# Kernel tuning notes

Measured on AMD Instinct MI355X. Metric: run time of the kernel, lower is better.

Reference implementation:

```python
import jax, jax.numpy as jnp
import numpy as np

N_NODES, N_EDGES, H = 25000, 400000, 64
EPS = 1e-15


def _norm(x):
    return jnp.sqrt(jnp.sum(x * x, axis=-1, keepdims=True))


def _projx(x, c):
    norm = _norm(x)
    max_norm = (1.0 - 1e-5) / jnp.sqrt(c)
    scale = jnp.minimum(max_norm / jnp.maximum(norm, EPS), 1.0)
    return x * scale


def _expmap0(x, c):
    norm = _norm(x)
    sc = jnp.sqrt(c)
    return jnp.tanh(sc * norm) * x / (norm * sc + EPS)


def _logmap0(x, c):
    norm = _norm(x)
    sc = jnp.sqrt(c)
    return (1.0 / sc) * jnp.arctanh(jnp.minimum(sc * norm, 1.0 - 1e-5)) * x / (norm + EPS)


def _mobius_add(x, y, c):
    x2 = jnp.sum(x * x, axis=-1, keepdims=True)
    y2 = jnp.sum(y * y, axis=-1, keepdims=True)
    xy = jnp.sum(x * y, axis=-1, keepdims=True)
    num = (1.0 + 2.0 * c * xy + c * y2) * x + (1.0 - c * x2) * y
    denom = 1.0 + 2.0 * c * xy + c * c * x2 * y2
    return num / (denom + EPS)


def _mobius_linear(x, W, b, c):
    t = _logmap0(x, c)
    out = t @ W.T + b
    return _expmap0(out, c)


def setup_inputs() -> dict:
    key = jax.random.key(0)
    ks = jax.random.split(key, 12)
    h_V = jax.random.normal(ks[0], (N_NODES, H), dtype=jnp.float32) * 0.3
    h_E = jax.random.normal(ks[1], (N_EDGES, 3 * H), dtype=jnp.float32) * 0.3
    src = jax.random.randint(ks[2], (N_EDGES,), 0, N_NODES, dtype=jnp.int32)
    dst = jax.random.randint(ks[3], (N_EDGES,), 0, N_NODES, dtype=jnp.int32)
    log_c = jnp.zeros((), dtype=jnp.float32)  # c = 1.0

    def lin(k, out_d, in_d):
        bound = 1.0 / np.sqrt(in_d)
        kw, kb = jax.random.split(k)
        W = jax.random.uniform(kw, (out_d, in_d), jnp.float32, -bound, bound)
        b = jax.random.uniform(kb, (out_d,), jnp.float32, -bound, bound)
        return W, b

    W1_w, W1_b = lin(ks[4], H, 5 * H)
    W2_w, W2_b = lin(ks[5], H, H)
    W3_w, W3_b = lin(ks[6], H, H)
    return {"h_V": h_V, "h_E": h_E, "src": src, "dst": dst, "log_c": log_c,
            "W1_w": W1_w, "W1_b": W1_b, "W2_w": W2_w, "W2_b": W2_b,
            "W3_w": W3_w, "W3_b": W3_b}


def reference(h_V, h_E, src, dst, log_c, W1_w, W1_b, W2_w, W2_b, W3_w, W3_b):
    c = jnp.exp(log_c)
    n_nodes = h_V.shape[0]
    h_E = _projx(h_E, c)
    h_V = _projx(h_V, c)
    # edge gather -> fused mobius-linear chain  [E, 5H] -> [E, H]
    h_EV = jnp.concatenate([h_E, h_V[src], h_V[dst]], axis=-1)
    h_EV = _mobius_linear(h_EV, W1_w, W1_b, c)
    h_EV = _mobius_linear(_projx(jax.nn.relu(h_EV), c), W2_w, W2_b, c)
    h_msg = _mobius_linear(_projx(jax.nn.relu(h_EV), c), W3_w, W3_b, c)
    # hyperbolic aggregate: logmap0 -> scatter-mean over src -> expmap0
    tangent = _logmap0(h_msg, c)
    sums = jax.ops.segment_sum(tangent, src, num_segments=n_nodes)
    counts = jax.ops.segment_sum(jnp.ones((tangent.shape[0],), tangent.dtype), src,
                                 num_segments=n_nodes)
    agg_t = sums / jnp.maximum(counts, 1.0)[:, None]
    agg = _expmap0(agg_t, c)
    h_V = _mobius_add(h_V, agg, c)  # dropout disabled (eval)
    return _projx(h_V, c)
```

## Files before the change

### kernel.cpp

```cpp
#include <hip/hip_runtime.h>
#include <hip/hip_bf16.h>
#include <math.h>

#define EPSF 1e-15f

typedef __attribute__((ext_vector_type(8))) short bf16x8;
typedef __attribute__((ext_vector_type(16))) float f32x16;

__device__ __forceinline__ unsigned short f2bf(float x) {
    unsigned u = __float_as_uint(x);
    u += 0x7fffu + ((u >> 16) & 1u);
    return (unsigned short)(u >> 16);
}
__device__ __forceinline__ float bf2f(unsigned short b) {
    return __uint_as_float(((unsigned)b) << 16);
}
__device__ __forceinline__ unsigned pkbf(float lo, float hi) {
    __hip_bfloat162 h = __float22bfloat162_rn(make_float2(lo, hi));
    return *reinterpret_cast<unsigned*>(&h);
}
__device__ __forceinline__ float fast_tanh_pos(float x) {
    if (x < 0.25f) { float x2 = x * x; return x * (1.0f - x2 * (0.33333334f - 0.13333334f * x2)); }
    float e = __expf(2.0f * x);
    return 1.0f - 2.0f / (e + 1.0f);
}
__device__ __forceinline__ float fast_atanh01(float y) {
    if (y < 0.125f) { float y2 = y * y; return y * (1.0f + y2 * (0.33333334f + 0.2f * y2)); }
    return 0.5f * __logf((1.0f + y) / (1.0f - y));
}

__device__ __forceinline__ float wred(float v) {
#pragma unroll
    for (int off = 32; off; off >>= 1) v += __shfl_xor(v, off);
    return v;
}

__global__ void prep_wfrag(const float* __restrict__ W1, const float* __restrict__ W2,
                           const float* __restrict__ W3, unsigned short* __restrict__ Wf) {
    int idx = blockIdx.x * blockDim.x + threadIdx.x;
    if (idx >= 56 * 64) return;
    int fid = idx >> 6, lane = idx & 63;
    int e31 = lane & 31, hi = lane >> 5;
    unsigned short* dstp = Wf + ((size_t)fid * 64 + lane) * 8;
    if (fid < 40) {
        int ks = fid >> 1, t = fid & 1;
        int n = 32 * t + e31;
        int k0 = 16 * ks + 8 * hi;
#pragma unroll
        for (int i = 0; i < 8; ++i) dstp[i] = f2bf(W1[n * 320 + k0 + i]);
    } else {
        const float* srcW = (fid < 48) ? W2 : W3;
        int b = (fid < 48) ? fid - 40 : fid - 48;
        int ks = b >> 1, t2 = b & 1;
        int n = 32 * t2 + e31;
        int cb = 32 * (ks >> 1) + 16 * (ks & 1) + 4 * hi;
#pragma unroll
        for (int i = 0; i < 8; ++i) dstp[i] = f2bf(srcW[n * 64 + cb + 8 * (i >> 2) + (i & 3)]);
    }
}

__global__ void __launch_bounds__(256)
node_prep(const float* __restrict__ hV, const float* __restrict__ logc,
          unsigned short* __restrict__ hVp, float* __restrict__ pj, int n_nodes) {
    int wid  = (blockIdx.x * blockDim.x + threadIdx.x) >> 6;
    int lane = threadIdx.x & 63;
    if (wid >= n_nodes) return;
    float c    = __expf(logc[0]);
    float scq  = sqrtf(c);
    float maxn = (1.0f - 1e-5f) / scq;
    float x = hV[(size_t)wid * 64 + lane];
    float p = wred(x * x);
    float sS = fminf(maxn / fmaxf(sqrtf(p), EPSF), 1.0f);
    hVp[(size_t)wid * 64 + lane] = f2bf(x * sS);
    if (lane == 0) pj[wid] = sS * sS * p;
}

__global__ void hist_kernel(const int* __restrict__ src, int* __restrict__ cnt,
                            int* __restrict__ slot, int n_edges) {
    int e = blockIdx.x * blockDim.x + threadIdx.x;
    if (e < n_edges) slot[e] = atomicAdd(&cnt[src[e]], 1);
}

__global__ void __launch_bounds__(1024)
scan_rowptr(const int* __restrict__ cnt, int* __restrict__ rowptr, int n) {
    __shared__ int wpart[16];
    int C   = (n + 1023) >> 10;
    int tid = threadIdx.x;
    int beg = tid * C;
    int end = beg + C; if (end > n) end = n;
    int s = 0;
    if (beg < n) for (int k = beg; k < end; ++k) s += cnt[k];
    int lane = tid & 63, wv = tid >> 6;
    int v = s;
#pragma unroll
    for (int off = 1; off < 64; off <<= 1) {
        int t = __shfl_up(v, off);
        if (lane >= off) v += t;
    }
    if (lane == 63) wpart[wv] = v;
    __syncthreads();
    if (tid < 64) {
        int t = (tid < 16) ? wpart[tid] : 0;
#pragma unroll
        for (int off = 1; off < 16; off <<= 1) {
            int u = __shfl_up(t, off);
            if (lane >= off) t += u;
        }
        if (tid < 16) wpart[tid] = t;
    }
    __syncthreads();
    int base = (wv ? wpart[wv - 1] : 0) + (v - s);
    if (beg < n) {
        int run = base;
        for (int k = beg; k < end; ++k) { rowptr[k] = run; run += cnt[k]; }
    }
    if (tid == 1023) rowptr[n] = wpart[15];
}

__global__ void slotfix_kernel(const int* __restrict__ src, const int* __restrict__ rowptr,
                               int* __restrict__ slot, int n_edges) {
    int e = blockIdx.x * blockDim.x + threadIdx.x;
    if (e < n_edges) slot[e] += rowptr[src[e]];
}

__device__ __forceinline__ void stage_mlp32(float (&v)[2][16],
                                            const unsigned short* WfL, int fbase,
                                            const float* __restrict__ bvec,
                                            float scq, float maxn, int lane, int hi) {
    float n2 = 0.f, rn2 = 0.f;
    float u[2][16];
#pragma unroll
    for (int t = 0; t < 2; ++t)
#pragma unroll
        for (int j = 0; j < 16; ++j) {
            float x = v[t][j];
            n2 = fmaf(x, x, n2);
            float y = fmaxf(x, 0.f);
            u[t][j] = y;
            rn2 = fmaf(y, y, rn2);
        }
    n2  += __shfl_xor(n2, 32);
    rn2 += __shfl_xor(rn2, 32);
    float n  = sqrtf(n2);
    float h  = fast_tanh_pos(scq * n) / (n * scq + EPSF);
    float rn = h * sqrtf(rn2);
    float ps = fminf(maxn / fmaxf(rn, EPSF), 1.0f);
    float pn = rn * ps;
    float gg = fast_atanh01(fminf(scq * pn, 1.0f - 1e-5f)) / (scq * (pn + EPSF));
    float f2 = h * ps * gg;

    f32x16 acc[2] = {};
#pragma unroll
    for (int ks = 0; ks < 4; ++ks) {
        int t = ks >> 1, jb = 8 * (ks & 1);
        union { bf16x8 b; unsigned w[4]; } B;
        B.w[0] = pkbf(u[t][jb + 0], u[t][jb + 1]);
        B.w[1] = pkbf(u[t][jb + 2], u[t][jb + 3]);
        B.w[2] = pkbf(u[t][jb + 4], u[t][jb + 5]);
        B.w[3] = pkbf(u[t][jb + 6], u[t][jb + 7]);
#pragma unroll
        for (int t2 = 0; t2 < 2; ++t2) {
            bf16x8 wf = *reinterpret_cast<const bf16x8*>(
                &WfL[((fbase + ks * 2 + t2) * 64 + lane) * 8]);
            acc[t2] = __builtin_amdgcn_mfma_f32_32x32x16_bf16(wf, B.b, acc[t2], 0, 0, 0);
        }
    }
#pragma unroll
    for (int t2 = 0; t2 < 2; ++t2)
#pragma unroll
        for (int q = 0; q < 4; ++q) {
            const float4 bv = *reinterpret_cast<const float4*>(&bvec[32 * t2 + 8 * q + 4 * hi]);
            v[t2][4 * q + 0] = fmaf(f2, acc[t2][4 * q + 0], bv.x);
            v[t2][4 * q + 1] = fmaf(f2, acc[t2][4 * q + 1], bv.y);
            v[t2][4 * q + 2] = fmaf(f2, acc[t2][4 * q + 2], bv.z);
            v[t2][4 * q + 3] = fmaf(f2, acc[t2][4 * q + 3], bv.w);
        }
}

__global__ void __launch_bounds__(256, 2)
edge_mfma(const float* __restrict__ hE, const int* __restrict__ src,
          const int* __restrict__ dst, const float* __restrict__ logc,
          const unsigned short* __restrict__ Wf, const unsigned short* __restrict__ hVp,
          const float* __restrict__ pj,
          const float* __restrict__ b1, const float* __restrict__ b2,
          const float* __restrict__ b3, const int* __restrict__ slot,
          unsigned short* __restrict__ tg, int n_edges) {
    __shared__ __align__(16) unsigned short WfL[28672];
    {
        const uint4* wsrc = reinterpret_cast<const uint4*>(Wf);
        uint4* wdst = reinterpret_cast<uint4*>(WfL);
#pragma unroll
        for (int i = 0; i < 14; ++i)
            wdst[i * 256 + threadIdx.x] = wsrc[i * 256 + threadIdx.x];
    }
    __syncthreads();

    int lane = threadIdx.x & 63;
    int w    = threadIdx.x >> 6;
    int tile = blockIdx.x * 4 + w;
    int e0 = tile * 32;
    if (e0 >= n_edges) return;

    float c    = __expf(logc[0]);
    float scq  = sqrtf(c);
    float maxn = (1.0f - 1e-5f) / scq;

    int e31 = lane & 31, hi = lane >> 5;
    int ev = e0 + e31; if (ev >= n_edges) ev = n_edges - 1;
    int s16 = src[ev], d16 = dst[ev];
    float pjS = pj[s16], pjD = pj[d16];
    int sl = slot[ev];

    float4 ha[24];
    const float* eb = hE + (size_t)ev * 192 + 8 * hi;
#pragma unroll
    for (int ks = 0; ks < 12; ++ks) {
        const float4* p4 = reinterpret_cast<const float4*>(eb + 16 * ks);
        ha[2 * ks]     = p4[0];
        ha[2 * ks + 1] = p4[1];
    }
    const bf16x8* vsp = reinterpret_cast<const bf16x8*>(hVp + (size_t)s16 * 64);
    const bf16x8* vdp = reinterpret_cast<const bf16x8*>(hVp + (size_t)d16 * 64);
    bf16x8 aS[4], aD[4];
#pragma unroll
    for (int q = 0; q < 4; ++q) { aS[q] = vsp[2 * q + hi]; aD[q] = vdp[2 * q + hi]; }

    f32x16 accE[2] = {}, accV[2] = {};
    float pE = 0.f;
#pragma unroll
    for (int ks = 0; ks < 12; ++ks) {
        float4 a0 = ha[2 * ks], a1 = ha[2 * ks + 1];
        pE += a0.x*a0.x + a0.y*a0.y + a0.z*a0.z + a0.w*a0.w
            + a1.x*a1.x + a1.y*a1.y + a1.z*a1.z + a1.w*a1.w;
        union { bf16x8 b; unsigned u[4]; } cv;
        cv.u[0] = pkbf(a0.x, a0.y);
        cv.u[1] = pkbf(a0.z, a0.w);
        cv.u[2] = pkbf(a1.x, a1.y);
        cv.u[3] = pkbf(a1.z, a1.w);
#pragma unroll
        for (int t = 0; t < 2; ++t) {
            bf16x8 wf = *reinterpret_cast<const bf16x8*>(&WfL[((ks * 2 + t) * 64 + lane) * 8]);
            accE[t] = __builtin_amdgcn_mfma_f32_32x32x16_bf16(wf, cv.b, accE[t], 0, 0, 0);
        }
    }
#pragma unroll
    for (int q = 0; q < 4; ++q) {
#pragma unroll
        for (int t = 0; t < 2; ++t) {
            bf16x8 wf = *reinterpret_cast<const bf16x8*>(&WfL[(((12 + q) * 2 + t) * 64 + lane) * 8]);
            accV[t] = __builtin_amdgcn_mfma_f32_32x32x16_bf16(wf, aS[q], accV[t], 0, 0, 0);
        }
    }
#pragma unroll
    for (int q = 0; q < 4; ++q) {
#pragma unroll
        for (int t = 0; t < 2; ++t) {
            bf16x8 wf = *reinterpret_cast<const bf16x8*>(&WfL[(((16 + q) * 2 + t) * 64 + lane) * 8]);
            accV[t] = __builtin_amdgcn_mfma_f32_32x32x16_bf16(wf, aD[q], accV[t], 0, 0, 0);
        }
    }

    pE += __shfl_xor(pE, 32);
    float sE = fminf(maxn / fmaxf(sqrtf(pE), EPSF), 1.0f);
    float nt = sqrtf(sE * sE * pE + pjS + pjD);
    float gq = fast_atanh01(fminf(scq * nt, 1.0f - 1e-5f)) / (scq * (nt + EPSF));

    float v[2][16];
#pragma unroll
    for (int t = 0; t < 2; ++t)
#pragma unroll
        for (int q = 0; q < 4; ++q) {
            const float4 bv = *reinterpret_cast<const float4*>(&b1[32 * t + 8 * q + 4 * hi]);
            v[t][4*q+0] = fmaf(gq, fmaf(sE, accE[t][4*q+0], accV[t][4*q+0]), bv.x);
            v[t][4*q+1] = fmaf(gq, fmaf(sE, accE[t][4*q+1], accV[t][4*q+1]), bv.y);
            v[t][4*q+2] = fmaf(gq, fmaf(sE, accE[t][4*q+2], accV[t][4*q+2]), bv.z);
            v[t][4*q+3] = fmaf(gq, fmaf(sE, accE[t][4*q+3], accV[t][4*q+3]), bv.w);
        }

    stage_mlp32(v, WfL, 40, b2, scq, maxn, lane, hi);
    stage_mlp32(v, WfL, 48, b3, scq, maxn, lane, hi);

    float n2 = 0.f;
#pragma unroll
    for (int t = 0; t < 2; ++t)
#pragma unroll
        for (int j = 0; j < 16; ++j) n2 = fmaf(v[t][j], v[t][j], n2);
    n2 += __shfl_xor(n2, 32);
    float n  = sqrtf(n2);
    float h  = fast_tanh_pos(scq * n) / (n * scq + EPSF);
    float hn = h * n;
    float g4 = fast_atanh01(fminf(scq * hn, 1.0f - 1e-5f)) / (scq * (hn + EPSF));
    float fT = g4 * h;

    if (e0 + e31 < n_edges) {
        unsigned short* orow = tg + (size_t)sl * 64;
#pragma unroll
        for (int t = 0; t < 2; ++t)
#pragma unroll
            for (int q = 0; q < 4; ++q) {
                uint2 o;
                o.x = pkbf(fT * v[t][4*q+0], fT * v[t][4*q+1]);
                o.y = pkbf(fT * v[t][4*q+2], fT * v[t][4*q+3]);
                *reinterpret_cast<uint2*>(&orow[32 * t + 8 * q + 4 * hi]) = o;
            }
    }
}

__global__ void __launch_bounds__(256)
node_gather(const float* __restrict__ hV, const float* __restrict__ logc,
            const unsigned short* __restrict__ tg, const int* __restrict__ rowptr,
            float* __restrict__ out, int n_nodes) {
    int wid  = (blockIdx.x * blockDim.x + threadIdx.x) >> 6;
    int lane = threadIdx.x & 63;
    if (wid >= n_nodes) return;

    float c    = __expf(logc[0]);
    float scq  = sqrtf(c);
    float maxn = (1.0f - 1e-5f) / scq;

    int beg = rowptr[wid], end = rowptr[wid + 1];
    int g = lane >> 4, i15 = lane & 15;
    float s0 = 0.f, s1 = 0.f, s2 = 0.f, s3 = 0.f;
    for (int i = beg + g; i < end; i += 4) {
        uint2 p = *reinterpret_cast<const uint2*>(&tg[(size_t)i * 64 + i15 * 4]);
        s0 += bf2f((unsigned short)(p.x & 0xffff));
        s1 += bf2f((unsigned short)(p.x >> 16));
        s2 += bf2f((unsigned short)(p.y & 0xffff));
        s3 += bf2f((unsigned short)(p.y >> 16));
    }
    s0 += __shfl_xor(s0, 16); s0 += __shfl_xor(s0, 32);
    s1 += __shfl_xor(s1, 16); s1 += __shfl_xor(s1, 32);
    s2 += __shfl_xor(s2, 16); s2 += __shfl_xor(s2, 32);
    s3 += __shfl_xor(s3, 16); s3 += __shfl_xor(s3, 32);
    int srcl = lane >> 2;
    float a0 = __shfl(s0, srcl), a1 = __shfl(s1, srcl);
    float a2 = __shfl(s2, srcl), a3 = __shfl(s3, srcl);
    float ssum = (lane & 2) ? ((lane & 1) ? a3 : a2) : ((lane & 1) ? a1 : a0);

    float inv = 1.f / fmaxf((float)(end - beg), 1.f);
    float at  = ssum * inv;

    float an2 = wred(at * at);
    float an  = sqrtf(an2);
    float ae  = fast_tanh_pos(scq * an) / (an * scq + EPSF);

    float xv  = hV[(size_t)wid * 64 + lane];
    float hs2 = wred(xv * xv);
    float sX  = fminf(maxn / fmaxf(sqrtf(hs2), EPSF), 1.0f);

    float x = sX * xv, y = ae * at;
    float x2 = wred(x * x);
    float y2 = wred(y * y);
    float xy = wred(x * y);

    float ca = 1.f + 2.f * c * xy + c * y2;
    float cb = 1.f - c * x2;
    float id = 1.f / (1.f + 2.f * c * xy + c * c * x2 * y2 + EPSF);

    float r   = (ca * x + cb * y) * id;
    float rn2 = wred(r * r);
    float rs  = fminf(maxn / fmaxf(sqrtf(rn2), EPSF), 1.0f);

    out[(size_t)wid * 64 + lane] = rs * r;
}

extern "C" void kernel_launch(void* const* d_in, const int* in_sizes, int n_in,
                              void* d_out, int out_size, void* d_ws, size_t ws_size,
                              hipStream_t stream) {
    const float* hV   = (const float*)d_in[0];
    const float* hE   = (const float*)d_in[1];
    const int*   src  = (const int*)d_in[2];
    const int*   dst  = (const int*)d_in[3];
    const float* logc = (const float*)d_in[4];
    const float* W1   = (const float*)d_in[5];
    const float* b1   = (const float*)d_in[6];
    const float* W2   = (const float*)d_in[7];
    const float* b2   = (const float*)d_in[8];
    const float* W3   = (const float*)d_in[9];
    const float* b3   = (const float*)d_in[10];

    int n_nodes = in_sizes[0] / 64;
    int n_edges = in_sizes[2];
    float* out = (float*)d_out;

    char* wsb = (char*)d_ws;
    unsigned short* Wf = (unsigned short*)wsb;
    size_t off = 56 * 512 * sizeof(unsigned short);
    int* cnt    = (int*)(wsb + off);   off += (size_t)n_nodes * 4;
    int* rowptr = (int*)(wsb + off);   off += (size_t)(n_nodes + 1) * 4;
    int* slot   = (int*)(wsb + off);   off += (size_t)n_edges * 4;
    float* pj   = (float*)(wsb + off); off += (size_t)n_nodes * 4;
    off = (off + 15) & ~(size_t)15;
    unsigned short* hVp = (unsigned short*)(wsb + off);
    off += (size_t)n_nodes * 64 * 2;
    off = (off + 15) & ~(size_t)15;
    unsigned short* tg = (unsigned short*)(wsb + off);

    hipMemsetAsync(cnt, 0, (size_t)n_nodes * sizeof(int), stream);

    prep_wfrag<<<(56 * 64 + 255) / 256, 256, 0, stream>>>(W1, W2, W3, Wf);
    node_prep<<<(n_nodes + 3) / 4, 256, 0, stream>>>(hV, logc, hVp, pj, n_nodes);
    hist_kernel<<<(n_edges + 255) / 256, 256, 0, stream>>>(src, cnt, slot, n_edges);
    scan_rowptr<<<1, 1024, 0, stream>>>(cnt, rowptr, n_nodes);
    slotfix_kernel<<<(n_edges + 255) / 256, 256, 0, stream>>>(src, rowptr, slot, n_edges);

    int tiles = (n_edges + 31) / 32;
    edge_mfma<<<(tiles + 3) / 4, 256, 0, stream>>>(
        hE, src, dst, logc, Wf, hVp, pj, b1, b2, b3, slot, tg, n_edges);

    node_gather<<<(n_nodes + 3) / 4, 256, 0, stream>>>(
        hV, logc, tg, rowptr, out, n_nodes);
}
```

Measured before the change: 220.9 us.

## Make edge kernel persistent with software-pipelined prefetch of next tile

Measured after the change: 295.8 us. 33.9% more time.

```diff
diff --git a/kernel.cpp b/kernel.cpp
--- a/kernel.cpp
+++ b/kernel.cpp
@@ -184,7 +184,7 @@
           const float* __restrict__ pj,
           const float* __restrict__ b1, const float* __restrict__ b2,
           const float* __restrict__ b3, const int* __restrict__ slot,
-          unsigned short* __restrict__ tg, int n_edges) {
+          unsigned short* __restrict__ tg, int n_edges, int n_tiles) {
     __shared__ __align__(16) unsigned short WfL[28672];
     {
         const uint4* wsrc = reinterpret_cast<const uint4*>(Wf);
@@ -197,112 +197,144 @@
 
     int lane = threadIdx.x & 63;
     int w    = threadIdx.x >> 6;
-    int tile = blockIdx.x * 4 + w;
-    int e0 = tile * 32;
-    if (e0 >= n_edges) return;
+    int e31 = lane & 31, hi = lane >> 5;
 
     float c    = __expf(logc[0]);
     float scq  = sqrtf(c);
     float maxn = (1.0f - 1e-5f) / scq;
 
-    int e31 = lane & 31, hi = lane >> 5;
-    int ev = e0 + e31; if (ev >= n_edges) ev = n_edges - 1;
+    int wstride = gridDim.x * 4;
+    int tile = blockIdx.x * 4 + w;
+    if (tile >= n_tiles) return;
+
+    int ev = tile * 32 + e31; if (ev >= n_edges) ev = n_edges - 1;
     int s16 = src[ev], d16 = dst[ev];
+    int sl  = slot[ev];
+    float4 ha[24];
+    {
+        const float* eb = hE + (size_t)ev * 192 + 8 * hi;
+#pragma unroll
+        for (int ks = 0; ks < 12; ++ks) {
+            const float4* p4 = reinterpret_cast<const float4*>(eb + 16 * ks);
+            ha[2 * ks]     = p4[0];
+            ha[2 * ks + 1] = p4[1];
+        }
+    }
+    bf16x8 aS[4], aD[4];
+    {
+        const bf16x8* vsp = reinterpret_cast<const bf16x8*>(hVp + (size_t)s16 * 64);
+        const bf16x8* vdp = reinterpret_cast<const bf16x8*>(hVp + (size_t)d16 * 64);
+#pragma unroll
+        for (int q = 0; q < 4; ++q) { aS[q] = vsp[2 * q + hi]; aD[q] = vdp[2 * q + hi]; }
+    }
     float pjS = pj[s16], pjD = pj[d16];
-    int sl = slot[ev];
-
-    float4 ha[24];
-    const float* eb = hE + (size_t)ev * 192 + 8 * hi;
-#pragma unroll
-    for (int ks = 0; ks < 12; ++ks) {
-        const float4* p4 = reinterpret_cast<const float4*>(eb + 16 * ks);
-        ha[2 * ks]     = p4[0];
-        ha[2 * ks + 1] = p4[1];
-    }
-    const bf16x8* vsp = reinterpret_cast<const bf16x8*>(hVp + (size_t)s16 * 64);
-    const bf16x8* vdp = reinterpret_cast<const bf16x8*>(hVp + (size_t)d16 * 64);
-    bf16x8 aS[4], aD[4];
-#pragma unroll
-    for (int q = 0; q < 4; ++q) { aS[q] = vsp[2 * q + hi]; aD[q] = vdp[2 * q + hi]; }
-
-    f32x16 accE[2] = {}, accV[2] = {};
-    float pE = 0.f;
-#pragma unroll
-    for (int ks = 0; ks < 12; ++ks) {
-        float4 a0 = ha[2 * ks], a1 = ha[2 * ks + 1];
-        pE += a0.x*a0.x + a0.y*a0.y + a0.z*a0.z + a0.w*a0.w
-            + a1.x*a1.x + a1.y*a1.y + a1.z*a1.z + a1.w*a1.w;
-        union { bf16x8 b; unsigned u[4]; } cv;
-        cv.u[0] = pkbf(a0.x, a0.y);
-        cv.u[1] = pkbf(a0.z, a0.w);
-        cv.u[2] = pkbf(a1.x, a1.y);
-        cv.u[3] = pkbf(a1.z, a1.w);
-#pragma unroll
-        for (int t = 0; t < 2; ++t) {
-            bf16x8 wf = *reinterpret_cast<const bf16x8*>(&WfL[((ks * 2 + t) * 64 + lane) * 8]);
-            accE[t] = __builtin_amdgcn_mfma_f32_32x32x16_bf16(wf, cv.b, accE[t], 0, 0, 0);
-        }
-    }
-#pragma unroll
-    for (int q = 0; q < 4; ++q) {
-#pragma unroll
-        for (int t = 0; t < 2; ++t) {
-            bf16x8 wf = *reinterpret_cast<const bf16x8*>(&WfL[(((12 + q) * 2 + t) * 64 + lane) * 8]);
-            accV[t] = __builtin_amdgcn_mfma_f32_32x32x16_bf16(wf, aS[q], accV[t], 0, 0, 0);
-        }
-    }
-#pragma unroll
-    for (int q = 0; q < 4; ++q) {
-#pragma unroll
-        for (int t = 0; t < 2; ++t) {
-            bf16x8 wf = *reinterpret_cast<const bf16x8*>(&WfL[(((16 + q) * 2 + t) * 64 + lane) * 8]);
-            accV[t] = __builtin_amdgcn_mfma_f32_32x32x16_bf16(wf, aD[q], accV[t], 0, 0, 0);
-        }
-    }
-
-    pE += __shfl_xor(pE, 32);
-    float sE = fminf(maxn / fmaxf(sqrtf(pE), EPSF), 1.0f);
-    float nt = sqrtf(sE * sE * pE + pjS + pjD);
-    float gq = fast_atanh01(fminf(scq * nt, 1.0f - 1e-5f)) / (scq * (nt + EPSF));
-
-    float v[2][16];
-#pragma unroll
-    for (int t = 0; t < 2; ++t)
+
+    for (;;) {
+        f32x16 accE[2] = {}, accV[2] = {};
+        float pE = 0.f;
+#pragma unroll
+        for (int ks = 0; ks < 12; ++ks) {
+            float4 a0 = ha[2 * ks], a1 = ha[2 * ks + 1];
+            pE += a0.x*a0.x + a0.y*a0.y + a0.z*a0.z + a0.w*a0.w
+                + a1.x*a1.x + a1.y*a1.y + a1.z*a1.z + a1.w*a1.w;
+            union { bf16x8 b; unsigned u[4]; } cv;
+            cv.u[0] = pkbf(a0.x, a0.y);
+            cv.u[1] = pkbf(a0.z, a0.w);
+            cv.u[2] = pkbf(a1.x, a1.y);
+            cv.u[3] = pkbf(a1.z, a1.w);
+#pragma unroll
+            for (int t = 0; t < 2; ++t) {
+                bf16x8 wf = *reinterpret_cast<const bf16x8*>(&WfL[((ks * 2 + t) * 64 + lane) * 8]);
+                accE[t] = __builtin_amdgcn_mfma_f32_32x32x16_bf16(wf, cv.b, accE[t], 0, 0, 0);
+            }
+        }
 #pragma unroll
         for (int q = 0; q < 4; ++q) {
-            const float4 bv = *reinterpret_cast<const float4*>(&b1[32 * t + 8 * q + 4 * hi]);
-            v[t][4*q+0] = fmaf(gq, fmaf(sE, accE[t][4*q+0], accV[t][4*q+0]), bv.x);
-            v[t][4*q+1] = fmaf(gq, fmaf(sE, accE[t][4*q+1], accV[t][4*q+1]), bv.y);
-            v[t][4*q+2] = fmaf(gq, fmaf(sE, accE[t][4*q+2], accV[t][4*q+2]), bv.z);
-            v[t][4*q+3] = fmaf(gq, fmaf(sE, accE[t][4*q+3], accV[t][4*q+3]), bv.w);
-        }
-
-    stage_mlp32(v, WfL, 40, b2, scq, maxn, lane, hi);
-    stage_mlp32(v, WfL, 48, b3, scq, maxn, lane, hi);
-
-    float n2 = 0.f;
-#pragma unroll
-    for (int t = 0; t < 2; ++t)
-#pragma unroll
-        for (int j = 0; j < 16; ++j) n2 = fmaf(v[t][j], v[t][j], n2);
-    n2 += __shfl_xor(n2, 32);
-    float n  = sqrtf(n2);
-    float h  = fast_tanh_pos(scq * n) / (n * scq + EPSF);
-    float hn = h * n;
-    float g4 = fast_atanh01(fminf(scq * hn, 1.0f - 1e-5f)) / (scq * (hn + EPSF));
-    float fT = g4 * h;
-
-    if (e0 + e31 < n_edges) {
-        unsigned short* orow = tg + (size_t)sl * 64;
+#pragma unroll
+            for (int t = 0; t < 2; ++t) {
+                bf16x8 wf = *reinterpret_cast<const bf16x8*>(&WfL[(((12 + q) * 2 + t) * 64 + lane) * 8]);
+                accV[t] = __builtin_amdgcn_mfma_f32_32x32x16_bf16(wf, aS[q], accV[t], 0, 0, 0);
+            }
+        }
+#pragma unroll
+        for (int q = 0; q < 4; ++q) {
+#pragma unroll
+            for (int t = 0; t < 2; ++t) {
+                bf16x8 wf = *reinterpret_cast<const bf16x8*>(&WfL[(((16 + q) * 2 + t) * 64 + lane) * 8]);
+                accV[t] = __builtin_amdgcn_mfma_f32_32x32x16_bf16(wf, aD[q], accV[t], 0, 0, 0);
+            }
+        }
+
+        pE += __shfl_xor(pE, 32);
+        float sE = fminf(maxn / fmaxf(sqrtf(pE), EPSF), 1.0f);
+        float nt = sqrtf(sE * sE * pE + pjS + pjD);
+        float gq = fast_atanh01(fminf(scq * nt, 1.0f - 1e-5f)) / (scq * (nt + EPSF));
+
+        float v[2][16];
 #pragma unroll
         for (int t = 0; t < 2; ++t)
 #pragma unroll
             for (int q = 0; q < 4; ++q) {
-                uint2 o;
-                o.x = pkbf(fT * v[t][4*q+0], fT * v[t][4*q+1]);
-                o.y = pkbf(fT * v[t][4*q+2], fT * v[t][4*q+3]);
-                *reinterpret_cast<uint2*>(&orow[32 * t + 8 * q + 4 * hi]) = o;
+                const float4 bv = *reinterpret_cast<const float4*>(&b1[32 * t + 8 * q + 4 * hi]);
+                v[t][4*q+0] = fmaf(gq, fmaf(sE, accE[t][4*q+0], accV[t][4*q+0]), bv.x);
+                v[t][4*q+1] = fmaf(gq, fmaf(sE, accE[t][4*q+1], accV[t][4*q+1]), bv.y);
+                v[t][4*q+2] = fmaf(gq, fmaf(sE, accE[t][4*q+2], accV[t][4*q+2]), bv.z);
+                v[t][4*q+3] = fmaf(gq, fmaf(sE, accE[t][4*q+3], accV[t][4*q+3]), bv.w);
             }
+
+        int  sl_cur = sl;
+        bool wr     = (tile * 32 + e31) < n_edges;
+
+        int tile2 = tile + wstride;
+        bool more = tile2 < n_tiles;
+        if (more) {
+            ev = tile2 * 32 + e31; if (ev >= n_edges) ev = n_edges - 1;
+            s16 = src[ev]; d16 = dst[ev]; sl = slot[ev];
+            const float* eb = hE + (size_t)ev * 192 + 8 * hi;
+#pragma unroll
+            for (int ks = 0; ks < 12; ++ks) {
+                const float4* p4 = reinterpret_cast<const float4*>(eb + 16 * ks);
+                ha[2 * ks]     = p4[0];
+                ha[2 * ks + 1] = p4[1];
+            }
+            const bf16x8* vsp = reinterpret_cast<const bf16x8*>(hVp + (size_t)s16 * 64);
+            const bf16x8* vdp = reinterpret_cast<const bf16x8*>(hVp + (size_t)d16 * 64);
+#pragma unroll
+            for (int q = 0; q < 4; ++q) { aS[q] = vsp[2 * q + hi]; aD[q] = vdp[2 * q + hi]; }
+            pjS = pj[s16]; pjD = pj[d16];
+        }
+        __builtin_amdgcn_sched_barrier(0);
+
+        stage_mlp32(v, WfL, 40, b2, scq, maxn, lane, hi);
+        stage_mlp32(v, WfL, 48, b3, scq, maxn, lane, hi);
+
+        float n2 = 0.f;
+#pragma unroll
+        for (int t = 0; t < 2; ++t)
+#pragma unroll
+            for (int j = 0; j < 16; ++j) n2 = fmaf(v[t][j], v[t][j], n2);
+        n2 += __shfl_xor(n2, 32);
+        float n  = sqrtf(n2);
+        float h  = fast_tanh_pos(scq * n) / (n * scq + EPSF);
+        float hn = h * n;
+        float g4 = fast_atanh01(fminf(scq * hn, 1.0f - 1e-5f)) / (scq * (hn + EPSF));
+        float fT = g4 * h;
+
+        if (wr) {
+            unsigned short* orow = tg + (size_t)sl_cur * 64;
+#pragma unroll
+            for (int t = 0; t < 2; ++t)
+#pragma unroll
+                for (int q = 0; q < 4; ++q) {
+                    uint2 o;
+                    o.x = pkbf(fT * v[t][4*q+0], fT * v[t][4*q+1]);
+                    o.y = pkbf(fT * v[t][4*q+2], fT * v[t][4*q+3]);
+                    *reinterpret_cast<uint2*>(&orow[32 * t + 8 * q + 4 * hi]) = o;
+                }
+        }
+
+        if (!more) break;
+        tile = tile2;
     }
 }
 
@@ -404,9 +436,11 @@
     scan_rowptr<<<1, 1024, 0, stream>>>(cnt, rowptr, n_nodes);
     slotfix_kernel<<<(n_edges + 255) / 256, 256, 0, stream>>>(src, rowptr, slot, n_edges);
 
-    int tiles = (n_edges + 31) / 32;
-    edge_mfma<<<(tiles + 3) / 4, 256, 0, stream>>>(
-        hE, src, dst, logc, Wf, hVp, pj, b1, b2, b3, slot, tg, n_edges);
+    int n_tiles = (n_edges + 31) / 32;
+    int nblocks = (n_tiles + 3) / 4;
+    if (nblocks > 512) nblocks = 512;
+    edge_mfma<<<nblocks, 256, 0, stream>>>(
+        hE, src, dst, logc, Wf, hVp, pj, b1, b2, b3, slot, tg, n_edges, n_tiles);
 
     node_gather<<<(n_nodes + 3) / 4, 256, 0, stream>>>(
         hV, logc, tg, rowptr, out, n_nodes);
```

## Split edge-feature GEMM into separate kernel and fold slotfix into edge kernel

Applied to the files above, without the earlier changes.

Result: slower. 526.5 us (+138.3%).

```diff
diff --git a/kernel.cpp b/kernel.cpp
--- a/kernel.cpp
+++ b/kernel.cpp
@@ -117,10 +117,52 @@
     if (tid == 1023) rowptr[n] = wpart[15];
 }
 
-__global__ void slotfix_kernel(const int* __restrict__ src, const int* __restrict__ rowptr,
-                               int* __restrict__ slot, int n_edges) {
-    int e = blockIdx.x * blockDim.x + threadIdx.x;
-    if (e < n_edges) slot[e] += rowptr[src[e]];
+__global__ void __launch_bounds__(256, 8)
+gemm1e(const float* __restrict__ hE, const unsigned short* __restrict__ Wf,
+       unsigned short* __restrict__ yEb, float* __restrict__ pEarr,
+       int n_edges, int n_tiles) {
+    int lane = threadIdx.x & 63;
+    int w    = threadIdx.x >> 6;
+    int tile = blockIdx.x * 4 + w;
+    if (tile >= n_tiles) return;
+    int e31 = lane & 31, hi = lane >> 5;
+    int ev = tile * 32 + e31; if (ev >= n_edges) ev = n_edges - 1;
+
+    const bf16x8* Wfrag = reinterpret_cast<const bf16x8*>(Wf);
+    const float* eb = hE + (size_t)ev * 192 + 8 * hi;
+
+    f32x16 acc[2] = {};
+    float pE = 0.f;
+#pragma unroll
+    for (int ks = 0; ks < 12; ++ks) {
+        const float4* p4 = reinterpret_cast<const float4*>(eb + 16 * ks);
+        float4 a0 = p4[0], a1 = p4[1];
+        pE += a0.x*a0.x + a0.y*a0.y + a0.z*a0.z + a0.w*a0.w
+            + a1.x*a1.x + a1.y*a1.y + a1.z*a1.z + a1.w*a1.w;
+        union { bf16x8 b; unsigned u[4]; } cv;
+        cv.u[0] = pkbf(a0.x, a0.y);
+        cv.u[1] = pkbf(a0.z, a0.w);
+        cv.u[2] = pkbf(a1.x, a1.y);
+        cv.u[3] = pkbf(a1.z, a1.w);
+#pragma unroll
+        for (int t = 0; t < 2; ++t)
+            acc[t] = __builtin_amdgcn_mfma_f32_32x32x16_bf16(
+                Wfrag[(size_t)(ks * 2 + t) * 64 + lane], cv.b, acc[t], 0, 0, 0);
+    }
+    pE += __shfl_xor(pE, 32);
+
+    unsigned pk[16];
+#pragma unroll
+    for (int t = 0; t < 2; ++t)
+#pragma unroll
+        for (int wd = 0; wd < 8; ++wd)
+            pk[t * 8 + wd] = pkbf(acc[t][2 * wd], acc[t][2 * wd + 1]);
+    uint4* op = reinterpret_cast<uint4*>(yEb + ((size_t)tile * 64 + lane) * 32);
+    op[0] = make_uint4(pk[0],  pk[1],  pk[2],  pk[3]);
+    op[1] = make_uint4(pk[4],  pk[5],  pk[6],  pk[7]);
+    op[2] = make_uint4(pk[8],  pk[9],  pk[10], pk[11]);
+    op[3] = make_uint4(pk[12], pk[13], pk[14], pk[15]);
+    if (hi == 0 && tile * 32 + e31 < n_edges) pEarr[tile * 32 + e31] = pE;
 }
 
 __device__ __forceinline__ void stage_mlp32(float (&v)[2][16],
@@ -177,20 +219,22 @@
         }
 }
 
-__global__ void __launch_bounds__(256, 2)
-edge_mfma(const float* __restrict__ hE, const int* __restrict__ src,
-          const int* __restrict__ dst, const float* __restrict__ logc,
+__global__ void __launch_bounds__(256, 4)
+edge_mfma(const unsigned short* __restrict__ yEb, const float* __restrict__ pEarr,
+          const int* __restrict__ src, const int* __restrict__ dst,
+          const float* __restrict__ logc,
           const unsigned short* __restrict__ Wf, const unsigned short* __restrict__ hVp,
           const float* __restrict__ pj,
           const float* __restrict__ b1, const float* __restrict__ b2,
-          const float* __restrict__ b3, const int* __restrict__ slot,
-          unsigned short* __restrict__ tg, int n_edges) {
-    __shared__ __align__(16) unsigned short WfL[28672];
+          const float* __restrict__ b3, const int* __restrict__ slot_,
+          const int* __restrict__ rowptr,
+          unsigned short* __restrict__ tg, int n_edges, int n_tiles) {
+    __shared__ __align__(16) unsigned short WfL[16384];
     {
-        const uint4* wsrc = reinterpret_cast<const uint4*>(Wf);
+        const uint4* wsrc = reinterpret_cast<const uint4*>(Wf) + 1536;
         uint4* wdst = reinterpret_cast<uint4*>(WfL);
 #pragma unroll
-        for (int i = 0; i < 14; ++i)
+        for (int i = 0; i < 8; ++i)
             wdst[i * 256 + threadIdx.x] = wsrc[i * 256 + threadIdx.x];
     }
     __syncthreads();
@@ -198,69 +242,48 @@
     int lane = threadIdx.x & 63;
     int w    = threadIdx.x >> 6;
     int tile = blockIdx.x * 4 + w;
-    int e0 = tile * 32;
-    if (e0 >= n_edges) return;
+    if (tile >= n_tiles) return;
 
     float c    = __expf(logc[0]);
     float scq  = sqrtf(c);
     float maxn = (1.0f - 1e-5f) / scq;
 
     int e31 = lane & 31, hi = lane >> 5;
-    int ev = e0 + e31; if (ev >= n_edges) ev = n_edges - 1;
+    int ev = tile * 32 + e31; if (ev >= n_edges) ev = n_edges - 1;
     int s16 = src[ev], d16 = dst[ev];
+    int sl = slot_[ev] + rowptr[s16];
     float pjS = pj[s16], pjD = pj[d16];
-    int sl = slot[ev];
-
-    float4 ha[24];
-    const float* eb = hE + (size_t)ev * 192 + 8 * hi;
-#pragma unroll
-    for (int ks = 0; ks < 12; ++ks) {
-        const float4* p4 = reinterpret_cast<const float4*>(eb + 16 * ks);
-        ha[2 * ks]     = p4[0];
-        ha[2 * ks + 1] = p4[1];
-    }
+    float pE  = pEarr[ev];
+
+    const uint4* yp = reinterpret_cast<const uint4*>(yEb + ((size_t)tile * 64 + lane) * 32);
+    uint4 y0 = yp[0], y1 = yp[1], y2 = yp[2], y3 = yp[3];
+    unsigned yw[16] = { y0.x, y0.y, y0.z, y0.w, y1.x, y1.y, y1.z, y1.w,
+                        y2.x, y2.y, y2.z, y2.w, y3.x, y3.y, y3.z, y3.w };
+
     const bf16x8* vsp = reinterpret_cast<const bf16x8*>(hVp + (size_t)s16 * 64);
     const bf16x8* vdp = reinterpret_cast<const bf16x8*>(hVp + (size_t)d16 * 64);
     bf16x8 aS[4], aD[4];
 #pragma unroll
     for (int q = 0; q < 4; ++q) { aS[q] = vsp[2 * q + hi]; aD[q] = vdp[2 * q + hi]; }
 
-    f32x16 accE[2] = {}, accV[2] = {};
-    float pE = 0.f;
-#pragma unroll
-    for (int ks = 0; ks < 12; ++ks) {
-        float4 a0 = ha[2 * ks], a1 = ha[2 * ks + 1];
-        pE += a0.x*a0.x + a0.y*a0.y + a0.z*a0.z + a0.w*a0.w
-            + a1.x*a1.x + a1.y*a1.y + a1.z*a1.z + a1.w*a1.w;
-        union { bf16x8 b; unsigned u[4]; } cv;
-        cv.u[0] = pkbf(a0.x, a0.y);
-        cv.u[1] = pkbf(a0.z, a0.w);
-        cv.u[2] = pkbf(a1.x, a1.y);
-        cv.u[3] = pkbf(a1.z, a1.w);
+    f32x16 accV[2] = {};
+#pragma unroll
+    for (int q = 0; q < 4; ++q) {
 #pragma unroll
         for (int t = 0; t < 2; ++t) {
-            bf16x8 wf = *reinterpret_cast<const bf16x8*>(&WfL[((ks * 2 + t) * 64 + lane) * 8]);
-            accE[t] = __builtin_amdgcn_mfma_f32_32x32x16_bf16(wf, cv.b, accE[t], 0, 0, 0);
+            bf16x8 wf = *reinterpret_cast<const bf16x8*>(&WfL[((q * 2 + t) * 64 + lane) * 8]);
+            accV[t] = __builtin_amdgcn_mfma_f32_32x32x16_bf16(wf, aS[q], accV[t], 0, 0, 0);
         }
     }
 #pragma unroll
     for (int q = 0; q < 4; ++q) {
 #pragma unroll
         for (int t = 0; t < 2; ++t) {
-            bf16x8 wf = *reinterpret_cast<const bf16x8*>(&WfL[(((12 + q) * 2 + t) * 64 + lane) * 8]);
-            accV[t] = __builtin_amdgcn_mfma_f32_32x32x16_bf16(wf, aS[q], accV[t], 0, 0, 0);
-        }
-    }
-#pragma unroll
-    for (int q = 0; q < 4; ++q) {
-#pragma unroll
-        for (int t = 0; t < 2; ++t) {
-            bf16x8 wf = *reinterpret_cast<const bf16x8*>(&WfL[(((16 + q) * 2 + t) * 64 + lane) * 8]);
+            bf16x8 wf = *reinterpret_cast<const bf16x8*>(&WfL[((8 + q * 2 + t) * 64 + lane) * 8]);
             accV[t] = __builtin_amdgcn_mfma_f32_32x32x16_bf16(wf, aD[q], accV[t], 0, 0, 0);
         }
     }
 
-    pE += __shfl_xor(pE, 32);
     float sE = fminf(maxn / fmaxf(sqrtf(pE), EPSF), 1.0f);
     float nt = sqrtf(sE * sE * pE + pjS + pjD);
     float gq = fast_atanh01(fminf(scq * nt, 1.0f - 1e-5f)) / (scq * (nt + EPSF));
@@ -271,14 +294,17 @@
 #pragma unroll
         for (int q = 0; q < 4; ++q) {
             const float4 bv = *reinterpret_cast<const float4*>(&b1[32 * t + 8 * q + 4 * hi]);
-            v[t][4*q+0] = fmaf(gq, fmaf(sE, accE[t][4*q+0], accV[t][4*q+0]), bv.x);
-            v[t][4*q+1] = fmaf(gq, fmaf(sE, accE[t][4*q+1], accV[t][4*q+1]), bv.y);
-            v[t][4*q+2] = fmaf(gq, fmaf(sE, accE[t][4*q+2], accV[t][4*q+2]), bv.z);
-            v[t][4*q+3] = fmaf(gq, fmaf(sE, accE[t][4*q+3], accV[t][4*q+3]), bv.w);
-        }
-
-    stage_mlp32(v, WfL, 40, b2, scq, maxn, lane, hi);
-    stage_mlp32(v, WfL, 48, b3, scq, maxn, lane, hi);
+#pragma unroll
+            for (int j = 0; j < 4; ++j) {
+                int f = t * 16 + q * 4 + j;
+                float ye = bf2f((unsigned short)(yw[f >> 1] >> (16 * (f & 1))));
+                float bb = (j == 0) ? bv.x : (j == 1) ? bv.y : (j == 2) ? bv.z : bv.w;
+                v[t][q * 4 + j] = fmaf(gq, fmaf(sE, ye, accV[t][q * 4 + j]), bb);
+            }
+        }
+
+    stage_mlp32(v, WfL, 16, b2, scq, maxn, lane, hi);
+    stage_mlp32(v, WfL, 24, b3, scq, maxn, lane, hi);
 
     float n2 = 0.f;
 #pragma unroll
@@ -292,7 +318,7 @@
     float g4 = fast_atanh01(fminf(scq * hn, 1.0f - 1e-5f)) / (scq * (hn + EPSF));
     float fT = g4 * h;
 
-    if (e0 + e31 < n_edges) {
+    if (tile * 32 + e31 < n_edges) {
         unsigned short* orow = tg + (size_t)sl * 64;
 #pragma unroll
         for (int t = 0; t < 2; ++t)
@@ -381,6 +407,7 @@
 
     int n_nodes = in_sizes[0] / 64;
     int n_edges = in_sizes[2];
+    int n_tiles = (n_edges + 31) / 32;
     float* out = (float*)d_out;
 
     char* wsb = (char*)d_ws;
@@ -390,10 +417,14 @@
     int* rowptr = (int*)(wsb + off);   off += (size_t)(n_nodes + 1) * 4;
     int* slot   = (int*)(wsb + off);   off += (size_t)n_edges * 4;
     float* pj   = (float*)(wsb + off); off += (size_t)n_nodes * 4;
+    float* pEarr= (float*)(wsb + off); off += (size_t)n_edges * 4;
     off = (off + 15) & ~(size_t)15;
     unsigned short* hVp = (unsigned short*)(wsb + off);
     off += (size_t)n_nodes * 64 * 2;
     off = (off + 15) & ~(size_t)15;
+    unsigned short* yEb = (unsigned short*)(wsb + off);
+    off += (size_t)n_tiles * 64 * 32 * 2;
+    off = (off + 15) & ~(size_t)15;
     unsigned short* tg = (unsigned short*)(wsb + off);
 
     hipMemsetAsync(cnt, 0, (size_t)n_nodes * sizeof(int), stream);
@@ -402,11 +433,12 @@
     node_prep<<<(n_nodes + 3) / 4, 256, 0, stream>>>(hV, logc, hVp, pj, n_nodes);
     hist_kernel<<<(n_edges + 255) / 256, 256, 0, stream>>>(src, cnt, slot, n_edges);
     scan_rowptr<<<1, 1024, 0, stream>>>(cnt, rowptr, n_nodes);
-    slotfix_kernel<<<(n_edges + 255) / 256, 256, 0, stream>>>(src, rowptr, slot, n_edges);
-
-    int tiles = (n_edges + 31) / 32;
-    edge_mfma<<<(tiles + 3) / 4, 256, 0, stream>>>(
-        hE, src, dst, logc, Wf, hVp, pj, b1, b2, b3, slot, tg, n_edges);
+
+    gemm1e<<<(n_tiles + 3) / 4, 256, 0, stream>>>(hE, Wf, yEb, pEarr, n_edges, n_tiles);
+
+    edge_mfma<<<(n_tiles + 3) / 4, 256, 0, stream>>>(
+        yEb, pEarr, src, dst, logc, Wf, hVp, pj, b1, b2, b3, slot, rowptr,
+        tg, n_edges, n_tiles);
 
     node_gather<<<(n_nodes + 3) / 4, 256, 0, stream>>>(
         hV, logc, tg, rowptr, out, n_nodes);
```
